# Kernel optimization log

Measured on AMD Instinct MI355X. Metric: run time of the kernel, lower is better.

Reference implementation:

```python
import jax, jax.numpy as jnp
import numpy as np
from jax import lax

WINDOW_SIZE = 11
SIGMA = 1.5
C1 = 0.01 ** 2
C2 = 0.03 ** 2


def _gaussian_window_2d(window_size, sigma):
    # matches torch.linspace(-ws//2+1, ws//2, ws) -> integers -5..5 for ws=11
    lo = -(window_size // 2) + 1 if window_size % 2 == 0 else -(window_size // 2)
    xs = np.linspace(-(window_size // 2) + 1 - (0 if window_size % 2 else 0), window_size // 2, window_size)
    # For ws=11: -(-11//2)+... torch computes linspace(-ws//2+1, ws//2, ws) with Python floor div:
    start = -(window_size // 2) if False else (-window_size) // 2 + 1
    xs = np.linspace(start, window_size // 2, window_size)
    g = np.exp(-(xs ** 2) / (2.0 * sigma ** 2))
    g = g / g.sum()
    w2d = np.outer(g, g).astype(np.float32)  # [ws, ws]
    return w2d


def _depthwise_conv(x, w2d, channel):
    # x: [B, C, H, W]; depthwise 'SAME' conv with shared gaussian kernel
    kernel = jnp.broadcast_to(jnp.asarray(w2d)[None, None], (channel, 1, w2d.shape[0], w2d.shape[1]))
    return lax.conv_general_dilated(
        x, kernel, window_strides=(1, 1), padding='SAME',
        feature_group_count=channel,
        dimension_numbers=('NCHW', 'OIHW', 'NCHW'))


def setup_inputs() -> dict:
    key = jax.random.key(0)
    k1, k2 = jax.random.split(key)
    img1 = jax.random.uniform(k1, (16, 3, 512, 512), dtype=jnp.float32)
    img2 = jax.random.uniform(k2, (16, 3, 512, 512), dtype=jnp.float32)
    return {"img1": img1, "img2": img2}


def reference(img1, img2):
    channel = img1.shape[1]
    w2d = _gaussian_window_2d(WINDOW_SIZE, SIGMA)

    mu1 = _depthwise_conv(img1, w2d, channel)
    mu2 = _depthwise_conv(img2, w2d, channel)
    sigma1_sq = _depthwise_conv(img1 * img1, w2d, channel) - mu1 * mu1
    sigma2_sq = _depthwise_conv(img2 * img2, w2d, channel) - mu2 * mu2
    sigma12 = _depthwise_conv(img1 * img2, w2d, channel) - mu1 * mu2

    ssim_map = ((2 * mu1 * mu2 + C1) * (2 * sigma12 + C2)) / (
        (mu1 * mu1 + mu2 * mu2 + C1) * (sigma1_sq + sigma2_sq + C2))
    return ssim_map.mean()
```

## Files before the change

### kernel.cpp

```cpp
#include <hip/hip_runtime.h>
#include <cstdint>

#define IMG_H 512
#define IMG_W 512
#define ROW_BYTES (IMG_W * 4)
#define NPLANES 48
#define PLANE_SZ (IMG_H * IMG_W)
#define N_ELEM (NPLANES * PLANE_SZ)

#define TILE_W 48
#define TILE_H 32
#define GX 11
#define GY 16
#define NBLOCKS (GX * GY * NPLANES)
#define VPITCH 59

#define SSIM_C1 1e-4f
#define SSIM_C2 9e-4f

typedef int rsrc_t __attribute__((ext_vector_type(4)));
__device__ float
llvm_amdgcn_raw_buffer_load_fp32(rsrc_t srsrc, int voffset, int soffset,
                                 int glc_slc) __asm("llvm.amdgcn.raw.buffer.load.f32");

__device__ inline rsrc_t make_rsrc(const void* p, int bytes) {
    rsrc_t r;
    r.x = (int)(uint32_t)(uintptr_t)p;
    r.y = (int)((uintptr_t)p >> 32);
    r.z = bytes;
    r.w = 0x00020000;
    return r;
}

__global__ __launch_bounds__(256, 4) void ssim_tile_kernel(
    const float* __restrict__ img1, const float* __restrict__ img2,
    double* __restrict__ partials)
{
    __shared__ float4 vs[TILE_H][VPITCH];
    __shared__ double wred[4];

    const float gw[11] = {0.00102838f, 0.00759876f, 0.03600077f, 0.10936069f,
                          0.21300553f, 0.26601172f, 0.21300553f, 0.10936069f,
                          0.03600077f, 0.00759876f, 0.00102838f};

    const int tid  = threadIdx.x;
    const int lane = tid & 63;
    const int wv   = tid >> 6;
    const int ox = blockIdx.x * TILE_W;
    const int oy = blockIdx.y * TILE_H;

    const float* p1 = img1 + (size_t)blockIdx.z * PLANE_SZ;
    const float* p2 = img2 + (size_t)blockIdx.z * PLANE_SZ;
    const rsrc_t rr1 = make_rsrc(p1, PLANE_SZ * 4);
    const rsrc_t rr2 = make_rsrc(p2, PLANE_SZ * 4);

    {
        const int r0 = wv * 8;
        const int srow0 = __builtin_amdgcn_readfirstlane(oy + r0 - 5);
        const int gcol = ox + lane - 5;
        const int coff = ((unsigned)gcol < (unsigned)IMG_W) ? (gcol * 4) : 0x48000000;

        float xs[18], ys[18];
        #pragma unroll
        for (int i = 0; i < 18; ++i) {
            const int soff = (srow0 + i) * ROW_BYTES;
            xs[i] = llvm_amdgcn_raw_buffer_load_fp32(rr1, coff, soff, 0);
            ys[i] = llvm_amdgcn_raw_buffer_load_fp32(rr2, coff, soff, 0);
        }

        float4 acc[8];
        #pragma unroll
        for (int o = 0; o < 8; ++o) acc[o] = make_float4(0.f, 0.f, 0.f, 0.f);
        #pragma unroll
        for (int i = 0; i < 18; ++i) {
            const float s = xs[i] + ys[i], d = xs[i] - ys[i];
            const float s2 = s * s, d2 = d * d;
            #pragma unroll
            for (int o = 0; o < 8; ++o) {
                const int k = i - o;
                if (k >= 0 && k <= 10) {
                    const float w = gw[k];
                    acc[o].x = fmaf(w, s,  acc[o].x);
                    acc[o].y = fmaf(w, d,  acc[o].y);
                    acc[o].z = fmaf(w, s2, acc[o].z);
                    acc[o].w = fmaf(w, d2, acc[o].w);
                }
            }
        }
        if (lane < 58) {
            #pragma unroll
            for (int o = 0; o < 8; ++o) vs[r0 + o][lane] = acc[o];
        }
    }
    __syncthreads();

    float lsum = 0.f;
    {
        const int r  = tid >> 3;
        const int c0 = (tid & 7) * 6;
        float4 m[6];
        #pragma unroll
        for (int j = 0; j < 6; ++j) m[j] = make_float4(0.f, 0.f, 0.f, 0.f);
        #pragma unroll
        for (int t = 0; t < 16; ++t) {
            const float4 v = vs[r][c0 + t];
            #pragma unroll
            for (int j = 0; j < 6; ++j) {
                const int k = t - j;
                if (k >= 0 && k <= 10) {
                    const float w = gw[k];
                    m[j].x = fmaf(w, v.x, m[j].x);
                    m[j].y = fmaf(w, v.y, m[j].y);
                    m[j].z = fmaf(w, v.z, m[j].z);
                    m[j].w = fmaf(w, v.w, m[j].w);
                }
            }
        }
        #pragma unroll
        for (int j = 0; j < 6; ++j) {
            if (ox + c0 + j < IMG_W) {
                const float mus = m[j].x, mud = m[j].y;
                const float es2 = m[j].z, ed2 = m[j].w;
                const float a = mus * mus, b = mud * mud;
                const float num1 = (a - b) * 0.5f + SSIM_C1;
                const float den1 = (a + b) * 0.5f + SSIM_C1;
                const float num2 = (es2 - ed2 - (a - b)) * 0.5f + SSIM_C2;
                const float den2 = (es2 + ed2 - (a + b)) * 0.5f + SSIM_C2;
                lsum += (num1 * num2) * __builtin_amdgcn_rcpf(den1 * den2);
            }
        }
    }

    #pragma unroll
    for (int off = 32; off > 0; off >>= 1)
        lsum += __shfl_down(lsum, off, 64);
    if (lane == 0) wred[wv] = (double)lsum;
    __syncthreads();
    if (tid == 0) {
        const int bid = blockIdx.x + GX * (blockIdx.y + GY * blockIdx.z);
        partials[bid] = wred[0] + wred[1] + wred[2] + wred[3];
    }
}

__global__ __launch_bounds__(1024) void ssim_finalize_kernel(
    const double* __restrict__ partials, float* __restrict__ out)
{
    __shared__ double wred[16];
    const int tid  = threadIdx.x;
    const int lane = tid & 63;
    const int wv   = tid >> 6;
    double s = 0.0;
    #pragma unroll
    for (int i = 0; i < 9; ++i) {
        const int idx = tid + i * 1024;
        if (idx < NBLOCKS) s += partials[idx];
    }
    #pragma unroll
    for (int off = 32; off > 0; off >>= 1)
        s += __shfl_down(s, off, 64);
    if (lane == 0) wred[wv] = s;
    __syncthreads();
    if (wv == 0) {
        double v = (lane < 16) ? wred[lane] : 0.0;
        v += __shfl_down(v, 8, 64);
        v += __shfl_down(v, 4, 64);
        v += __shfl_down(v, 2, 64);
        v += __shfl_down(v, 1, 64);
        if (lane == 0) out[0] = (float)(v / (double)N_ELEM);
    }
}

extern "C" void kernel_launch(void* const* d_in, const int* in_sizes, int n_in,
                              void* d_out, int out_size, void* d_ws, size_t ws_size,
                              hipStream_t stream)
{
    const float* img1 = (const float*)d_in[0];
    const float* img2 = (const float*)d_in[1];
    double* partials  = (double*)d_ws;
    float* out        = (float*)d_out;

    dim3 grid(GX, GY, NPLANES);
    ssim_tile_kernel<<<grid, dim3(256), 0, stream>>>(img1, img2, partials);
    ssim_finalize_kernel<<<1, dim3(1024), 0, stream>>>(partials, out);
}
```

Before: 139.5 us.

## Process two vertical tiles per block and prefetch second tile during horizontal pass

```diff
diff --git a/kernel.cpp b/kernel.cpp
--- a/kernel.cpp
+++ b/kernel.cpp
@@ -11,8 +11,8 @@
 #define TILE_W 48
 #define TILE_H 32
 #define GX 11
-#define GY 16
-#define NBLOCKS (GX * GY * NPLANES)
+#define GYB 8
+#define NBLOCKS (GX * GYB * NPLANES)
 #define VPITCH 59
 
 #define SSIM_C1 1e-4f
@@ -46,89 +46,107 @@
     const int tid  = threadIdx.x;
     const int lane = tid & 63;
     const int wv   = tid >> 6;
-    const int ox = blockIdx.x * TILE_W;
-    const int oy = blockIdx.y * TILE_H;
+    const int ox  = blockIdx.x * TILE_W;
+    const int oy0 = blockIdx.y * (2 * TILE_H);
 
     const float* p1 = img1 + (size_t)blockIdx.z * PLANE_SZ;
     const float* p2 = img2 + (size_t)blockIdx.z * PLANE_SZ;
     const rsrc_t rr1 = make_rsrc(p1, PLANE_SZ * 4);
     const rsrc_t rr2 = make_rsrc(p2, PLANE_SZ * 4);
 
+    const int gcol = ox + lane - 5;
+    const int coff = (lane < 58 && (unsigned)gcol < (unsigned)IMG_W)
+                         ? (gcol * 4) : 0x48000000;
+
+    float xs[18], ys[18];
     {
-        const int r0 = wv * 8;
-        const int srow0 = __builtin_amdgcn_readfirstlane(oy + r0 - 5);
-        const int gcol = ox + lane - 5;
-        const int coff = ((unsigned)gcol < (unsigned)IMG_W) ? (gcol * 4) : 0x48000000;
-
-        float xs[18], ys[18];
+        const int srow0 = __builtin_amdgcn_readfirstlane(oy0 + wv * 8 - 5);
         #pragma unroll
         for (int i = 0; i < 18; ++i) {
             const int soff = (srow0 + i) * ROW_BYTES;
             xs[i] = llvm_amdgcn_raw_buffer_load_fp32(rr1, coff, soff, 0);
             ys[i] = llvm_amdgcn_raw_buffer_load_fp32(rr2, coff, soff, 0);
         }
-
-        float4 acc[8];
-        #pragma unroll
-        for (int o = 0; o < 8; ++o) acc[o] = make_float4(0.f, 0.f, 0.f, 0.f);
-        #pragma unroll
-        for (int i = 0; i < 18; ++i) {
-            const float s = xs[i] + ys[i], d = xs[i] - ys[i];
-            const float s2 = s * s, d2 = d * d;
-            #pragma unroll
-            for (int o = 0; o < 8; ++o) {
-                const int k = i - o;
-                if (k >= 0 && k <= 10) {
-                    const float w = gw[k];
-                    acc[o].x = fmaf(w, s,  acc[o].x);
-                    acc[o].y = fmaf(w, d,  acc[o].y);
-                    acc[o].z = fmaf(w, s2, acc[o].z);
-                    acc[o].w = fmaf(w, d2, acc[o].w);
+    }
+
+    float lsum = 0.f;
+    #pragma unroll
+    for (int ty = 0; ty < 2; ++ty) {
+        {
+            const int r0 = wv * 8;
+            float4 acc[8];
+            #pragma unroll
+            for (int o = 0; o < 8; ++o) acc[o] = make_float4(0.f, 0.f, 0.f, 0.f);
+            #pragma unroll
+            for (int i = 0; i < 18; ++i) {
+                const float s = xs[i] + ys[i], d = xs[i] - ys[i];
+                const float s2 = s * s, d2 = d * d;
+                #pragma unroll
+                for (int o = 0; o < 8; ++o) {
+                    const int k = i - o;
+                    if (k >= 0 && k <= 10) {
+                        const float w = gw[k];
+                        acc[o].x = fmaf(w, s,  acc[o].x);
+                        acc[o].y = fmaf(w, d,  acc[o].y);
+                        acc[o].z = fmaf(w, s2, acc[o].z);
+                        acc[o].w = fmaf(w, d2, acc[o].w);
+                    }
                 }
             }
-        }
-        if (lane < 58) {
-            #pragma unroll
-            for (int o = 0; o < 8; ++o) vs[r0 + o][lane] = acc[o];
-        }
-    }
-    __syncthreads();
-
-    float lsum = 0.f;
-    {
-        const int r  = tid >> 3;
-        const int c0 = (tid & 7) * 6;
-        float4 m[6];
-        #pragma unroll
-        for (int j = 0; j < 6; ++j) m[j] = make_float4(0.f, 0.f, 0.f, 0.f);
-        #pragma unroll
-        for (int t = 0; t < 16; ++t) {
-            const float4 v = vs[r][c0 + t];
+            if (lane < 58) {
+                #pragma unroll
+                for (int o = 0; o < 8; ++o) vs[r0 + o][lane] = acc[o];
+            }
+        }
+        __syncthreads();
+
+        if (ty == 0) {
+            const int srow1 =
+                __builtin_amdgcn_readfirstlane(oy0 + TILE_H + wv * 8 - 5);
+            #pragma unroll
+            for (int i = 0; i < 18; ++i) {
+                const int soff = (srow1 + i) * ROW_BYTES;
+                xs[i] = llvm_amdgcn_raw_buffer_load_fp32(rr1, coff, soff, 0);
+                ys[i] = llvm_amdgcn_raw_buffer_load_fp32(rr2, coff, soff, 0);
+            }
+        }
+
+        {
+            const int r  = tid >> 3;
+            const int c0 = (tid & 7) * 6;
+            float4 m[6];
+            #pragma unroll
+            for (int j = 0; j < 6; ++j) m[j] = make_float4(0.f, 0.f, 0.f, 0.f);
+            #pragma unroll
+            for (int t = 0; t < 16; ++t) {
+                const float4 v = vs[r][c0 + t];
+                #pragma unroll
+                for (int j = 0; j < 6; ++j) {
+                    const int k = t - j;
+                    if (k >= 0 && k <= 10) {
+                        const float w = gw[k];
+                        m[j].x = fmaf(w, v.x, m[j].x);
+                        m[j].y = fmaf(w, v.y, m[j].y);
+                        m[j].z = fmaf(w, v.z, m[j].z);
+                        m[j].w = fmaf(w, v.w, m[j].w);
+                    }
+                }
+            }
             #pragma unroll
             for (int j = 0; j < 6; ++j) {
-                const int k = t - j;
-                if (k >= 0 && k <= 10) {
-                    const float w = gw[k];
-                    m[j].x = fmaf(w, v.x, m[j].x);
-                    m[j].y = fmaf(w, v.y, m[j].y);
-                    m[j].z = fmaf(w, v.z, m[j].z);
-                    m[j].w = fmaf(w, v.w, m[j].w);
+                if (ox + c0 + j < IMG_W) {
+                    const float mus = m[j].x, mud = m[j].y;
+                    const float es2 = m[j].z, ed2 = m[j].w;
+                    const float a = mus * mus, b = mud * mud;
+                    const float num1 = (a - b) * 0.5f + SSIM_C1;
+                    const float den1 = (a + b) * 0.5f + SSIM_C1;
+                    const float num2 = (es2 - ed2 - (a - b)) * 0.5f + SSIM_C2;
+                    const float den2 = (es2 + ed2 - (a + b)) * 0.5f + SSIM_C2;
+                    lsum += (num1 * num2) * __builtin_amdgcn_rcpf(den1 * den2);
                 }
             }
         }
-        #pragma unroll
-        for (int j = 0; j < 6; ++j) {
-            if (ox + c0 + j < IMG_W) {
-                const float mus = m[j].x, mud = m[j].y;
-                const float es2 = m[j].z, ed2 = m[j].w;
-                const float a = mus * mus, b = mud * mud;
-                const float num1 = (a - b) * 0.5f + SSIM_C1;
-                const float den1 = (a + b) * 0.5f + SSIM_C1;
-                const float num2 = (es2 - ed2 - (a - b)) * 0.5f + SSIM_C2;
-                const float den2 = (es2 + ed2 - (a + b)) * 0.5f + SSIM_C2;
-                lsum += (num1 * num2) * __builtin_amdgcn_rcpf(den1 * den2);
-            }
-        }
+        if (ty == 0) __syncthreads();
     }
 
     #pragma unroll
@@ -137,7 +155,7 @@
     if (lane == 0) wred[wv] = (double)lsum;
     __syncthreads();
     if (tid == 0) {
-        const int bid = blockIdx.x + GX * (blockIdx.y + GY * blockIdx.z);
+        const int bid = blockIdx.x + GX * (blockIdx.y + GYB * blockIdx.z);
         partials[bid] = wred[0] + wred[1] + wred[2] + wred[3];
     }
 }
@@ -151,7 +169,7 @@
     const int wv   = tid >> 6;
     double s = 0.0;
     #pragma unroll
-    for (int i = 0; i < 9; ++i) {
+    for (int i = 0; i < 5; ++i) {
         const int idx = tid + i * 1024;
         if (idx < NBLOCKS) s += partials[idx];
     }
@@ -179,7 +197,7 @@
     double* partials  = (double*)d_ws;
     float* out        = (float*)d_out;
 
-    dim3 grid(GX, GY, NPLANES);
+    dim3 grid(GX, GYB, NPLANES);
     ssim_tile_kernel<<<grid, dim3(256), 0, stream>>>(img1, img2, partials);
     ssim_finalize_kernel<<<1, dim3(1024), 0, stream>>>(partials, out);
 }
```

Result: no change. 138.2 us (-0.9%).
